# Kernel optimization log

Measured on AMD Instinct MI355X. Metric: run time of the kernel, lower is better.

Reference implementation:

```python
import jax, jax.numpy as jnp
import numpy as np

# dims: B batch, CIN/COUT channels, K kernel, H/W spatial, S stride, P padding
B, CIN, COUT, K, H, W, S, P = 8, 16, 64, 3, 32, 32, 1, 1
ALPHA, R, N_EKV, VT, VD = 0.05625, 0.1, 1.5, 0.025, 0.1


def setup_inputs() -> dict:
    key = jax.random.key(0)
    k1, k2 = jax.random.split(key)
    x = jax.random.normal(k1, (B, CIN, H, W), dtype=jnp.float32)
    # torch init: uniform_(theta, 1.0, 8.0)
    theta = jax.random.uniform(k2, (COUT, CIN * K * K), dtype=jnp.float32, minval=1.0, maxval=8.0)
    scale = jnp.array(1.0, dtype=jnp.float32)
    return {"x": x, "theta": theta, "scale": scale}


def _unfold(x, k, s, p):
    # torch.nn.Unfold: patches flattened channel-major as (C, kh, kw)
    b, c, h, w = x.shape
    ho = (h + 2 * p - k) // s + 1
    wo = (w + 2 * p - k) // s + 1
    xp = jnp.pad(x, ((0, 0), (0, 0), (p, p), (p, p)))
    patches = jnp.stack(
        [xp[:, :, i:i + ho * s:s, j:j + wo * s:s] for i in range(k) for j in range(k)],
        axis=2,
    )  # (B, C, K*K, Ho, Wo)
    return patches.reshape(b, c * k * k, ho * wo), ho, wo


def _log1p_exp_stable_sq(a):
    # clamp to [-50, 20] then softplus; squared (EKV f)
    a = jnp.clip(a, -50.0, 20.0)
    sp = jnp.log1p(jnp.exp(a))
    return sp * sp


def reference(x, theta, scale):
    theta = jnp.clip(theta, 1.0, 8.0)  # mirrors theta.data.clamp_(1, 8)
    vg, ho, wo = _unfold(x, K, S, P)          # (B, Cin*K^2, L)
    vg = vg[:, None, :, :]                    # (B, 1, Cin*K^2, L)
    vth = theta[None, :, :, None]             # (1, Cout, Cin*K^2, 1)
    denom = 2.0 * N_EKV * VT
    term1 = _log1p_exp_stable_sq((vg - vth) / denom)
    term2 = _log1p_exp_stable_sq((vg - vth - VD) / denom)
    currents = jnp.clip(ALPHA * (term1 - term2), 0.0, None)
    i_k = jnp.sum(currents, axis=2)           # reduce over Cin*K^2 -> (B, Cout, L)
    v_out = i_k * R * scale
    return v_out.reshape(x.shape[0], COUT, ho, wo)
```

## Files before the change

### kernel.cpp

```cpp
#include <hip/hip_runtime.h>

#define BB 8
#define CIN 16
#define COUT 64
#define HH 32
#define WW 32
#define PH 34
#define PW 36
#define PPLANE (PH * PW)

#define SCALE_C 19.235933878519388f
#define K2E 0.26359713811472845f
#define B_HI 28.85390081777927f
#define WINLO_S (-13.849872392533959f)
#define OUT_CONST (0.4804530139182014f * 0.05625f * 0.1f)

#define EXP2F(x) __builtin_amdgcn_exp2f(x)
#define LOG2F(x) __builtin_amdgcn_logf(x)

#define NTH (COUT * CIN * 9)
#define PAD_ELEMS (BB * CIN * PPLANE)

__global__ __launch_bounds__(256) void init_kernel(const float* __restrict__ x,
                                                   const float* __restrict__ theta,
                                                   float* __restrict__ xp,
                                                   float* __restrict__ thp) {
    if (blockIdx.x < 612) {
        int idx = blockIdx.x * 256 + threadIdx.x;
        int c = idx / PPLANE;
        int r = idx - c * PPLANE;
        int y = r / PW;
        int xc = r - y * PW;
        float v = 0.0f;
        if (y >= 1 && y <= HH && xc >= 1 && xc <= WW) {
            v = x[c * (HH * WW) + (y - 1) * WW + (xc - 1)] * SCALE_C;
        }
        xp[idx] = v;
    } else {
        int i = (blockIdx.x - 612) * 256 + threadIdx.x;
        if (i < NTH) {
            thp[i] = fminf(fmaxf(theta[i], 1.0f), 8.0f) * SCALE_C;
        }
    }
}

__device__ __forceinline__ void load12(const float* __restrict__ p, float4* v) {
#pragma unroll
    for (int dy = 0; dy < 3; ++dy)
        __builtin_memcpy(&v[dy], p + dy * PW, 16);
}

__device__ __forceinline__ void compute9(const float4* v, const float* __restrict__ thp,
                                         float* acc) {
#pragma unroll
    for (int dy = 0; dy < 3; ++dy) {
        float row[3] = {v[dy].x, v[dy].y, v[dy].z};
#pragma unroll
        for (int dx = 0; dx < 3; ++dx) {
            float b1 = row[dx] - thp[dy * 3 + dx];
            if (__any(b1 > WINLO_S)) {
                float e1 = EXP2F(b1);
                float e2 = e1 * K2E;
                float l1 = fminf(LOG2F(1.0f + e1), B_HI);
                float l2 = fminf(LOG2F(1.0f + e2), B_HI);
                float a = acc[dx];
                a = fmaf(l1, l1, a);
                a = fmaf(-l2, l2, a);
                acc[dx] = a;
            }
        }
    }
}

__global__ __launch_bounds__(256, 8) void ekv_kernel(const float* __restrict__ xp,
                                                     const float* __restrict__ thp,
                                                     const float* __restrict__ scale,
                                                     float* __restrict__ out) {
    int bid = blockIdx.x;
    int b = bid & 7;
    int tile = (bid >> 3) & 3;
    int co = (bid >> 8) * 8 + ((bid >> 5) & 7);

    int t = threadIdx.x;
    int ow = t & 31;
    int oh = tile * 8 + (t >> 5);

    const float* thc = thp + co * (CIN * 9);
    const float* p0 = xp + (size_t)b * (CIN * PPLANE) + oh * PW + ow;

    float acc[3] = {0.0f, 0.0f, 0.0f};

    float4 va[3], vb[3];
    load12(p0, va);
#pragma unroll 1
    for (int cin = 0; cin < CIN; cin += 2) {
        load12(p0 + (cin + 1) * PPLANE, vb);
        compute9(va, thc + cin * 9, acc);
        int nc = cin + 2 < CIN ? cin + 2 : CIN - 1;
        load12(p0 + nc * PPLANE, va);
        compute9(vb, thc + (cin + 1) * 9, acc);
    }

    float sc = scale[0] * (OUT_CONST);
    out[(((size_t)b * COUT + co) * HH + oh) * WW + ow] =
        (acc[0] + acc[1] + acc[2]) * sc;
}

extern "C" void kernel_launch(void* const* d_in, const int* in_sizes, int n_in,
                              void* d_out, int out_size, void* d_ws, size_t ws_size,
                              hipStream_t stream) {
    const float* x = (const float*)d_in[0];
    const float* theta = (const float*)d_in[1];
    const float* scale = (const float*)d_in[2];
    float* out = (float*)d_out;

    float* thp = (float*)d_ws;
    float* xp = thp + NTH;
    (void)ws_size;

    init_kernel<<<612 + (NTH + 255) / 256, 256, 0, stream>>>(x, theta, xp, thp);
    ekv_kernel<<<BB * 4 * COUT, 256, 0, stream>>>(xp, thp, scale, out);
}
```

Measured before the change: 74.77 us.

## Compute two adjacent output pixels per thread reusing loaded input rows

Each thread now produces two horizontally adjacent outputs, reusing the fourth lane of the already-loaded float4 rows. It halves the block count, regroups blocks to 16 output channels and 16 rows, and writes results as float2. The aim is to amortize input loads, theta reads and loop overhead over more transcendental work. In exchange it lowers thread count and occupancy, and the merged wave-level skip test may evaluate taps that one pixel alone would skip.

```diff
diff --git a/kernel.cpp b/kernel.cpp
--- a/kernel.cpp
+++ b/kernel.cpp
@@ -19,7 +19,6 @@
 #define LOG2F(x) __builtin_amdgcn_logf(x)
 
 #define NTH (COUT * CIN * 9)
-#define PAD_ELEMS (BB * CIN * PPLANE)
 
 __global__ __launch_bounds__(256) void init_kernel(const float* __restrict__ x,
                                                    const float* __restrict__ theta,
@@ -50,60 +49,70 @@
         __builtin_memcpy(&v[dy], p + dy * PW, 16);
 }
 
-__device__ __forceinline__ void compute9(const float4* v, const float* __restrict__ thp,
-                                         float* acc) {
+__device__ __forceinline__ void eval_tap(float b1, float& acc) {
+    float e1 = EXP2F(b1);
+    float e2 = e1 * K2E;
+    float l1 = fminf(LOG2F(1.0f + e1), B_HI);
+    float l2 = fminf(LOG2F(1.0f + e2), B_HI);
+    acc = fmaf(l1, l1, acc);
+    acc = fmaf(-l2, l2, acc);
+}
+
+__device__ __forceinline__ void compute18(const float4* v, const float* __restrict__ thp,
+                                          float* acc0, float* acc1) {
 #pragma unroll
     for (int dy = 0; dy < 3; ++dy) {
-        float row[3] = {v[dy].x, v[dy].y, v[dy].z};
+        float c0 = v[dy].x, c1 = v[dy].y, c2 = v[dy].z, c3 = v[dy].w;
+        float p0[3] = {c0, c1, c2};
+        float p1[3] = {c1, c2, c3};
 #pragma unroll
         for (int dx = 0; dx < 3; ++dx) {
-            float b1 = row[dx] - thp[dy * 3 + dx];
-            if (__any(b1 > WINLO_S)) {
-                float e1 = EXP2F(b1);
-                float e2 = e1 * K2E;
-                float l1 = fminf(LOG2F(1.0f + e1), B_HI);
-                float l2 = fminf(LOG2F(1.0f + e2), B_HI);
-                float a = acc[dx];
-                a = fmaf(l1, l1, a);
-                a = fmaf(-l2, l2, a);
-                acc[dx] = a;
+            float th = thp[dy * 3 + dx];
+            float bm = fmaxf(p0[dx], p1[dx]) - th;
+            if (__any(bm > WINLO_S)) {
+                eval_tap(p0[dx] - th, acc0[dx]);
+                eval_tap(p1[dx] - th, acc1[dx]);
             }
         }
     }
 }
 
-__global__ __launch_bounds__(256, 8) void ekv_kernel(const float* __restrict__ xp,
+__global__ __launch_bounds__(256, 4) void ekv_kernel(const float* __restrict__ xp,
                                                      const float* __restrict__ thp,
                                                      const float* __restrict__ scale,
                                                      float* __restrict__ out) {
     int bid = blockIdx.x;
     int b = bid & 7;
-    int tile = (bid >> 3) & 3;
-    int co = (bid >> 8) * 8 + ((bid >> 5) & 7);
+    int tile = (bid >> 3) & 1;
+    int co = (bid >> 8) * 16 + ((bid >> 4) & 15);
 
     int t = threadIdx.x;
-    int ow = t & 31;
-    int oh = tile * 8 + (t >> 5);
+    int owp = (t & 15) * 2;
+    int oh = tile * 16 + (t >> 4);
 
     const float* thc = thp + co * (CIN * 9);
-    const float* p0 = xp + (size_t)b * (CIN * PPLANE) + oh * PW + ow;
+    const float* p0 = xp + (size_t)b * (CIN * PPLANE) + oh * PW + owp;
 
-    float acc[3] = {0.0f, 0.0f, 0.0f};
+    float acc0[3] = {0.0f, 0.0f, 0.0f};
+    float acc1[3] = {0.0f, 0.0f, 0.0f};
 
     float4 va[3], vb[3];
     load12(p0, va);
 #pragma unroll 1
     for (int cin = 0; cin < CIN; cin += 2) {
         load12(p0 + (cin + 1) * PPLANE, vb);
-        compute9(va, thc + cin * 9, acc);
+        compute18(va, thc + cin * 9, acc0, acc1);
         int nc = cin + 2 < CIN ? cin + 2 : CIN - 1;
         load12(p0 + nc * PPLANE, va);
-        compute9(vb, thc + (cin + 1) * 9, acc);
+        compute18(vb, thc + (cin + 1) * 9, acc0, acc1);
     }
 
     float sc = scale[0] * (OUT_CONST);
-    out[(((size_t)b * COUT + co) * HH + oh) * WW + ow] =
-        (acc[0] + acc[1] + acc[2]) * sc;
+    float2 st;
+    st.x = (acc0[0] + acc0[1] + acc0[2]) * sc;
+    st.y = (acc1[0] + acc1[1] + acc1[2]) * sc;
+    float2* op = (float2*)(out + ((((size_t)b * COUT + co) * HH + oh) * WW + owp));
+    *op = st;
 }
 
 extern "C" void kernel_launch(void* const* d_in, const int* in_sizes, int n_in,
@@ -119,5 +128,5 @@
     (void)ws_size;
 
     init_kernel<<<612 + (NTH + 255) / 256, 256, 0, stream>>>(x, theta, xp, thp);
-    ekv_kernel<<<BB * 4 * COUT, 256, 0, stream>>>(xp, thp, scale, out);
+    ekv_kernel<<<BB * 2 * COUT, 256, 0, stream>>>(xp, thp, scale, out);
 }
```

Measured after the change: 75.49 us. About the same (+1.0%).
